# Optimization experiments

Measured on AMD Instinct MI355X. Metric: run time of the kernel, lower is better.

The kernel has to match this reference:

```python
import jax, jax.numpy as jnp
import numpy as np
from jax import lax

DIM = 64
D_STATE = 16
D_CONV = 4
EXPAND = 2
D_INNER = EXPAND * DIM  # 128
EPS = 1e-3  # keras LayerNormalization default epsilon


def setup_inputs() -> dict:
    key = jax.random.key(0)
    ks = jax.random.split(key, 9)
    B, H, W, D = 2, 48, 48, 48
    x = jax.random.normal(ks[0], (B, H, W, D, DIM), dtype=jnp.float32)
    # Dense kernels (fan-in scaled), conv kernel is depthwise: [k, 1, d_inner]
    W_in = jax.random.normal(ks[1], (DIM, 2 * D_INNER), jnp.float32) / np.sqrt(DIM)
    conv_w = jax.random.normal(ks[2], (D_CONV, 1, D_INNER), jnp.float32) / np.sqrt(D_CONV)
    conv_b = jnp.zeros((D_INNER,), jnp.float32)
    W_x = jax.random.normal(ks[3], (D_INNER, D_STATE + D_INNER), jnp.float32) / np.sqrt(D_INNER)
    W_dt = jax.random.normal(ks[4], (D_INNER, D_INNER), jnp.float32) / np.sqrt(D_INNER)
    b_dt = jnp.zeros((D_INNER,), jnp.float32)
    W_out = jax.random.normal(ks[5], (D_INNER, DIM), jnp.float32) / np.sqrt(D_INNER)
    gamma = jnp.ones((DIM,), jnp.float32)
    beta = jnp.zeros((DIM,), jnp.float32)
    return {"x": x, "W_in": W_in, "conv_w": conv_w, "conv_b": conv_b,
            "W_x": W_x, "W_dt": W_dt, "b_dt": b_dt, "W_out": W_out,
            "gamma": gamma, "beta": beta}


def _layernorm(z, gamma, beta):
    mu = jnp.mean(z, axis=-1, keepdims=True)
    var = jnp.mean(jnp.square(z - mu), axis=-1, keepdims=True)
    return gamma * (z - mu) * lax.rsqrt(var + EPS) + beta


def reference(x, W_in, conv_w, conv_b, W_x, W_dt, b_dt, W_out, gamma, beta):
    B, H, W, D, C = x.shape
    L = H * W * D
    x_flat = x.reshape(B, L, C)                       # [B, L, C]
    x_and_res = x_flat @ W_in                         # [B, L, 2*d_inner]
    x_ssm, res = jnp.split(x_and_res, 2, axis=-1)     # each [B, L, d_inner]
    # depthwise Conv1D, kernel=4, TF 'same' padding (pad_left=1, pad_right=2)
    x_ssm = lax.conv_general_dilated(
        x_ssm, conv_w, window_strides=(1,), padding=[(1, 2)],
        dimension_numbers=("NWC", "WIO", "NWC"), feature_group_count=D_INNER) + conv_b
    x_ssm = jax.nn.silu(x_ssm)
    # simplified SSM: projections + softplus + cumulative-sum scan over L
    x_proj = x_ssm @ W_x                              # [B, L, d_state+d_inner]
    dt = jax.nn.softplus(x_ssm @ W_dt + b_dt)         # [B, L, d_inner]
    state = jnp.cumsum(x_proj[..., :D_INNER] * dt, axis=1)  # [B, L, d_inner]
    y = state * jax.nn.silu(res)                      # gated output
    out = (y @ W_out).reshape(B, H, W, D, C)
    return _layernorm(out + x, gamma, beta)
```

## Files before the change

### kernel.cpp

```cpp
#include <hip/hip_runtime.h>
#include <hip/hip_bf16.h>
#include <math.h>

#define L_LEN 110592
#define TILE 32
#define NT 3456
#define NCH 64
#define TPC 54
#define STRX 72
#define STRC 136
#define RESS 132

typedef float  floatx4 __attribute__((ext_vector_type(4)));
typedef short  short8  __attribute__((ext_vector_type(8)));
typedef short  short4v __attribute__((ext_vector_type(4)));

__device__ __forceinline__ float fast_silu(float v) {
    return v * __builtin_amdgcn_rcpf(1.f + __expf(-v));
}
__device__ __forceinline__ float fast_softplus(float d) {
    return fmaxf(d, 0.f) + __logf(1.f + __expf(-fabsf(d)));
}
__device__ __forceinline__ short f2bf(float f) {
    __hip_bfloat16 h = __float2bfloat16(f);
    return *reinterpret_cast<short*>(&h);
}
__device__ __forceinline__ float bf2f(short s) {
    __hip_bfloat16 h = *reinterpret_cast<__hip_bfloat16*>(&s);
    return __bfloat162float(h);
}
__device__ __forceinline__ short8 pack_bf8(float4 a, float4 b) {
    short8 r;
    r[0] = f2bf(a.x); r[1] = f2bf(a.y); r[2] = f2bf(a.z); r[3] = f2bf(a.w);
    r[4] = f2bf(b.x); r[5] = f2bf(b.y); r[6] = f2bf(b.z); r[7] = f2bf(b.w);
    return r;
}

__global__ __launch_bounds__(256) void kW_w(
    const float* __restrict__ W_in, const float* __restrict__ W_x,
    const float* __restrict__ W_dt, const float* __restrict__ W_out,
    __hip_bfloat16* __restrict__ wti, __hip_bfloat16* __restrict__ wpt,
    __hip_bfloat16* __restrict__ wtr, __hip_bfloat16* __restrict__ wot)
{
    const int t = threadIdx.x;
    for (int idx = t; idx < 128 * 64; idx += 256) {
        int n = idx >> 6, k = idx & 63;
        wti[idx] = __float2bfloat16(W_in[k * 256 + n]);
        wtr[idx] = __float2bfloat16(W_in[k * 256 + 128 + n]);
    }
    for (int idx = t; idx < 256 * 128; idx += 256) {
        int n = idx >> 7, k = idx & 127;
        float v = (n < 128) ? W_x[k * 144 + n] : W_dt[k * 128 + (n - 128)];
        wpt[idx] = __float2bfloat16(v);
    }
    for (int idx = t; idx < 64 * 128; idx += 256) {
        int n = idx >> 7, k = idx & 127;
        wot[idx] = __float2bfloat16(W_out[k * 64 + n]);
    }
}

__global__ __launch_bounds__(256, 8) void kA(
    const float* __restrict__ x,
    const __hip_bfloat16* __restrict__ wti,
    const __hip_bfloat16* __restrict__ wpt,
    const float* __restrict__ conv_w, const float* __restrict__ conv_b,
    const float* __restrict__ b_dt,
    __hip_bfloat16* __restrict__ s, float* __restrict__ sums)
{
    __shared__ __align__(16) __hip_bfloat16 xbf[48 * STRX];
    __shared__ __align__(16) __hip_bfloat16 xcb[32 * STRC];

    const int t = threadIdx.x;
    const int lane = t & 63;
    const int w = t >> 6;
    const int quad = lane >> 4;
    const int lr = lane & 15;
    const int tile = blockIdx.x;
    const int b = blockIdx.y;
    const int l0 = tile * TILE;

    for (int idx = t; idx < 384; idx += 256) {
        const int row = idx >> 3, c8 = (idx & 7) << 3;
        const long gr = (long)l0 - 1 + row;
        float4 u0 = {0.f, 0.f, 0.f, 0.f}, u1 = {0.f, 0.f, 0.f, 0.f};
        if (gr >= 0 && gr < L_LEN) {
            const float* xp = x + (((long)b * L_LEN + gr) << 6) + c8;
            u0 = ((const float4*)xp)[0];
            u1 = ((const float4*)xp)[1];
        }
        *(short8*)&xbf[row * STRX + c8] = pack_bf8(u0, u1);
    }
    __syncthreads();

    {
        floatx4 acc[3][2] = {};
        #pragma unroll
        for (int ks = 0; ks < 2; ++ks) {
            short8 bfr0 = *(const short8*)(wti + ((w * 32 + lr) << 6) + ks * 32 + quad * 8);
            short8 bfr1 = *(const short8*)(wti + ((w * 32 + 16 + lr) << 6) + ks * 32 + quad * 8);
            #pragma unroll
            for (int mt = 0; mt < 3; ++mt) {
                short8 afr = *(const short8*)&xbf[(mt * 16 + lr) * STRX + ks * 32 + quad * 8];
                acc[mt][0] = __builtin_amdgcn_mfma_f32_16x16x32_bf16(afr, bfr0, acc[mt][0], 0, 0, 0);
                acc[mt][1] = __builtin_amdgcn_mfma_f32_16x16x32_bf16(afr, bfr1, acc[mt][1], 0, 0, 0);
            }
        }
        const int srcLane = (((quad + 1) & 3) << 4) | lr;
        #pragma unroll
        for (int jj = 0; jj < 2; ++jj) {
            const int col = w * 32 + jj * 16 + lr;
            const float cw0 = conv_w[col],       cw1 = conv_w[128 + col];
            const float cw2 = conv_w[256 + col], cw3 = conv_w[384 + col];
            const float cb = conv_b[col];
            #pragma unroll
            for (int m = 0; m < 2; ++m) {
                float s0 = (quad == 0) ? acc[m + 1][jj][0] : acc[m][jj][0];
                float s1 = (quad == 0) ? acc[m + 1][jj][1] : acc[m][jj][1];
                float s2 = (quad == 0) ? acc[m + 1][jj][2] : acc[m][jj][2];
                const float e0 = __shfl(s0, srcLane);
                const float e1 = __shfl(s1, srcLane);
                const float e2 = __shfl(s2, srcLane);
                const float a0 = acc[m][jj][0], a1 = acc[m][jj][1];
                const float a2 = acc[m][jj][2], a3 = acc[m][jj][3];
                const int rb = m * 16 + quad * 4;
                xcb[(rb + 0) * STRC + col] =
                    __float2bfloat16(fast_silu(cb + cw0 * a0 + cw1 * a1 + cw2 * a2 + cw3 * a3));
                xcb[(rb + 1) * STRC + col] =
                    __float2bfloat16(fast_silu(cb + cw0 * a1 + cw1 * a2 + cw2 * a3 + cw3 * e0));
                xcb[(rb + 2) * STRC + col] =
                    __float2bfloat16(fast_silu(cb + cw0 * a2 + cw1 * a3 + cw2 * e0 + cw3 * e1));
                xcb[(rb + 3) * STRC + col] =
                    __float2bfloat16(fast_silu(cb + cw0 * a3 + cw1 * e0 + cw2 * e1 + cw3 * e2));
            }
        }
    }
    __syncthreads();

    {
        floatx4 accx[2][2] = {}, accd[2][2] = {};
        #pragma unroll
        for (int ks = 0; ks < 4; ++ks) {
            short8 afr[2];
            #pragma unroll
            for (int mt = 0; mt < 2; ++mt)
                afr[mt] = *(const short8*)&xcb[(mt * 16 + lr) * STRC + ks * 32 + quad * 8];
            #pragma unroll
            for (int j = 0; j < 2; ++j) {
                const int n = w * 32 + j * 16 + lr;
                short8 bx = *(const short8*)(wpt + (n << 7) + ks * 32 + quad * 8);
                short8 bd = *(const short8*)(wpt + ((n + 128) << 7) + ks * 32 + quad * 8);
                #pragma unroll
                for (int mt = 0; mt < 2; ++mt) {
                    accx[mt][j] = __builtin_amdgcn_mfma_f32_16x16x32_bf16(afr[mt], bx, accx[mt][j], 0, 0, 0);
                    accd[mt][j] = __builtin_amdgcn_mfma_f32_16x16x32_bf16(afr[mt], bd, accd[mt][j], 0, 0, 0);
                }
            }
        }
        const long tbase = ((long)b * NT + tile) << 7;
        float ps0 = 0.f, ps1 = 0.f;
        #pragma unroll
        for (int j = 0; j < 2; ++j) {
            const int col = w * 32 + j * 16 + lr;
            const float bdv = b_dt[col];
            __hip_bfloat16* sp = s + ((tbase + col) << 5) + quad * 4;
            float psl = 0.f;
            #pragma unroll
            for (int mt = 0; mt < 2; ++mt) {
                short4v pk;
                #pragma unroll
                for (int r = 0; r < 4; ++r) {
                    float dv = accd[mt][j][r] + bdv;
                    float sv = accx[mt][j][r] * fast_softplus(dv);
                    short h = f2bf(sv);
                    pk[r] = h;
                    psl += bf2f(h);
                }
                *(short4v*)(sp + mt * 16) = pk;
            }
            if (j == 0) ps0 = psl; else ps1 = psl;
        }
        ps0 += __shfl_xor(ps0, 16); ps0 += __shfl_xor(ps0, 32);
        ps1 += __shfl_xor(ps1, 16); ps1 += __shfl_xor(ps1, 32);
        const long sb = ((long)b * NT + tile) << 7;
        if (quad == 0)      sums[sb + w * 32 + lr] = ps0;
        else if (quad == 1) sums[sb + w * 32 + 16 + lr] = ps1;
    }
}

__global__ __launch_bounds__(256) void kB1(const float* __restrict__ sums,
                                           float* __restrict__ csum)
{
    __shared__ float ps[256];
    const int t = threadIdx.x;
    const int c = t & 127, h = t >> 7;
    const int ch = blockIdx.x, b = blockIdx.y;
    const long tb = ((long)b * NT + ch * TPC + h * 27) * 128 + c;
    float tot = 0.f;
    for (int j = 0; j < 27; j += 9) {
        float v[9];
        #pragma unroll
        for (int k = 0; k < 9; ++k) v[k] = sums[tb + (long)(j + k) * 128];
        #pragma unroll
        for (int k = 0; k < 9; ++k) tot += v[k];
    }
    ps[t] = tot;
    __syncthreads();
    if (t < 128) csum[((long)b * NCH + ch) * 128 + t] = ps[t] + ps[t + 128];
}

__global__ __launch_bounds__(256) void kB2(float* __restrict__ csum)
{
    const int t = threadIdx.x;
    const int c = t & 127, b = t >> 7;
    const long base = (long)b * NCH * 128 + c;
    float run = 0.f;
    for (int ch = 0; ch < NCH; ch += 8) {
        float v[8];
        #pragma unroll
        for (int k = 0; k < 8; ++k) v[k] = csum[base + (long)(ch + k) * 128];
        #pragma unroll
        for (int k = 0; k < 8; ++k) {
            csum[base + (long)(ch + k) * 128] = run;
            run += v[k];
        }
    }
}

__global__ __launch_bounds__(128) void kB3(float* __restrict__ sums,
                                           const float* __restrict__ csum)
{
    const int c = threadIdx.x;
    const int ch = blockIdx.x, b = blockIdx.y;
    float run = csum[((long)b * NCH + ch) * 128 + c];
    const long tb = ((long)b * NT + ch * TPC) * 128 + c;
    for (int j = 0; j < TPC; j += 9) {
        float v[9];
        #pragma unroll
        for (int k = 0; k < 9; ++k) v[k] = sums[tb + (long)(j + k) * 128];
        #pragma unroll
        for (int k = 0; k < 9; ++k) {
            sums[tb + (long)(j + k) * 128] = run;
            run += v[k];
        }
    }
}

__global__ __launch_bounds__(256, 6) void kC(
    const float* __restrict__ x,
    const __hip_bfloat16* __restrict__ wtr,
    const __hip_bfloat16* __restrict__ wot,
    const float* __restrict__ gamma, const float* __restrict__ beta,
    const __hip_bfloat16* __restrict__ s, const float* __restrict__ offs,
    float* __restrict__ out)
{
    __shared__ float resf[32 * RESS];
    __shared__ __align__(16) char ubuf[32 * STRC * 2];
    __shared__ float totbuf[256];

    __hip_bfloat16* const ybf = (__hip_bfloat16*)ubuf;
    __hip_bfloat16* const xbf = (__hip_bfloat16*)ubuf;

    const int t = threadIdx.x;
    const int lane = t & 63;
    const int w = t >> 6;
    const int quad = lane >> 4;
    const int lr = lane & 15;
    const int tile = blockIdx.x;
    const int b = blockIdx.y;
    const int l0 = tile * TILE;
    const long base = (long)b * L_LEN;

    {
        const int row = t >> 3, c8 = (t & 7) << 3;
        const float* xp = x + ((base + l0 + row) << 6) + c8;
        float4 u0 = ((const float4*)xp)[0], u1 = ((const float4*)xp)[1];
        *(short8*)&xbf[row * STRX + c8] = pack_bf8(u0, u1);
    }
    __syncthreads();

    {
        floatx4 acc[2][2] = {};
        #pragma unroll
        for (int ks = 0; ks < 2; ++ks) {
            short8 bfr0 = *(const short8*)(wtr + ((w * 32 + lr) << 6) + ks * 32 + quad * 8);
            short8 bfr1 = *(const short8*)(wtr + ((w * 32 + 16 + lr) << 6) + ks * 32 + quad * 8);
            #pragma unroll
            for (int mt = 0; mt < 2; ++mt) {
                short8 afr = *(const short8*)&xbf[(mt * 16 + lr) * STRX + ks * 32 + quad * 8];
                acc[mt][0] = __builtin_amdgcn_mfma_f32_16x16x32_bf16(afr, bfr0, acc[mt][0], 0, 0, 0);
                acc[mt][1] = __builtin_amdgcn_mfma_f32_16x16x32_bf16(afr, bfr1, acc[mt][1], 0, 0, 0);
            }
        }
        #pragma unroll
        for (int mt = 0; mt < 2; ++mt)
            #pragma unroll
            for (int j = 0; j < 2; ++j) {
                const int col = w * 32 + j * 16 + lr;
                #pragma unroll
                for (int r = 0; r < 4; ++r)
                    resf[(mt * 16 + quad * 4 + r) * RESS + col] = fast_silu(acc[mt][j][r]);
            }
    }
    __syncthreads();

    {
        const int c = t & 127, h = t >> 7;
        const __hip_bfloat16* sp = s + ((((long)b * NT + tile) << 7) + c) * 32 + h * 16;
        short8 sv0 = *(const short8*)sp;
        short8 sv1 = *(const short8*)(sp + 8);
        float pfx[16];
        float run = 0.f;
        #pragma unroll
        for (int i = 0; i < 8; ++i) { run += bf2f(sv0[i]); pfx[i] = run; }
        #pragma unroll
        for (int i = 0; i < 8; ++i) { run += bf2f(sv1[i]); pfx[8 + i] = run; }
        totbuf[t] = run;
        __syncthreads();
        float off = offs[((long)b * NT + tile) * 128 + c];
        if (h) off += totbuf[c];
        #pragma unroll
        for (int q = 0; q < 16; ++q)
            ybf[(h * 16 + q) * STRC + c] =
                __float2bfloat16(resf[(h * 16 + q) * RESS + c] * (off + pfx[q]));
    }
    __syncthreads();

    {
        float* zbuf = resf;
        floatx4 acc[2] = {};
        const int n = w * 16 + lr;
        #pragma unroll
        for (int ks = 0; ks < 4; ++ks) {
            short8 bfr = *(const short8*)(wot + (n << 7) + ks * 32 + quad * 8);
            #pragma unroll
            for (int mt = 0; mt < 2; ++mt) {
                short8 afr = *(const short8*)&ybf[(mt * 16 + lr) * STRC + ks * 32 + quad * 8];
                acc[mt] = __builtin_amdgcn_mfma_f32_16x16x32_bf16(afr, bfr, acc[mt], 0, 0, 0);
            }
        }
        __syncthreads();
        #pragma unroll
        for (int mt = 0; mt < 2; ++mt)
            #pragma unroll
            for (int r = 0; r < 4; ++r)
                zbuf[(mt * 16 + quad * 4 + r) * 68 + n] = acc[mt][r];
    }
    __syncthreads();

    {
        const float* zbuf = resf;
        const int d = t & 63;
        const int dg = t >> 6;
        const float g  = gamma[d];
        const float bt = beta[d];
        #pragma unroll 2
        for (int i = 0; i < 8; ++i) {
            int q = dg + 4 * i;
            float z = zbuf[q * 68 + d] + x[(base + l0 + q) * 64 + d];
            float zsum = z;
            #pragma unroll
            for (int off = 32; off > 0; off >>= 1) zsum += __shfl_xor(zsum, off);
            float mu = zsum * 0.015625f;
            float dz = z - mu;
            float vsum = dz * dz;
            #pragma unroll
            for (int off = 32; off > 0; off >>= 1) vsum += __shfl_xor(vsum, off);
            float inv = rsqrtf(vsum * 0.015625f + 1e-3f);
            out[(base + l0 + q) * 64 + d] = g * dz * inv + bt;
        }
    }
}

extern "C" void kernel_launch(void* const* d_in, const int* in_sizes, int n_in,
                              void* d_out, int out_size, void* d_ws, size_t ws_size,
                              hipStream_t stream) {
    const float* x      = (const float*)d_in[0];
    const float* W_in   = (const float*)d_in[1];
    const float* conv_w = (const float*)d_in[2];
    const float* conv_b = (const float*)d_in[3];
    const float* W_x    = (const float*)d_in[4];
    const float* W_dt   = (const float*)d_in[5];
    const float* b_dt   = (const float*)d_in[6];
    const float* W_out  = (const float*)d_in[7];
    const float* gamma  = (const float*)d_in[8];
    const float* beta   = (const float*)d_in[9];
    float* out = (float*)d_out;

    __hip_bfloat16* s    = (__hip_bfloat16*)d_ws;
    float*          sums = (float*)((char*)d_ws + 56623104);
    float*          csum = (float*)((char*)d_ws + 60162048);
    __hip_bfloat16* wti  = (__hip_bfloat16*)((char*)d_ws + 88477696);
    __hip_bfloat16* wpt  = (__hip_bfloat16*)((char*)d_ws + 88494080);
    __hip_bfloat16* wtr  = (__hip_bfloat16*)((char*)d_ws + 88559616);
    __hip_bfloat16* wot  = (__hip_bfloat16*)((char*)d_ws + 88576000);

    kW_w<<<1, 256, 0, stream>>>(W_in, W_x, W_dt, W_out, wti, wpt, wtr, wot);
    dim3 grid(NT, 2);
    kA<<<grid, 256, 0, stream>>>(x, wti, wpt, conv_w, conv_b, b_dt, s, sums);
    dim3 gridB(NCH, 2);
    kB1<<<gridB, 256, 0, stream>>>(sums, csum);
    kB2<<<1, 256, 0, stream>>>(csum);
    kB3<<<gridB, 128, 0, stream>>>(sums, csum);
    kC<<<grid, 256, 0, stream>>>(x, wtr, wot, gamma, beta, s, sums, out);
}
```

Baseline: 283.4 us.

## Fuse pipeline into single kernel with decoupled look-back scan across tiles

Replaces the multi-kernel pipeline (projection kernel, three scan-offset kernels, output kernel) with one fused kernel. Each tile publishes its per-channel aggregate and, via flags, an inclusive prefix that later tiles read using a decoupled look-back. This removes the global round-trip of the bf16 state tensor and the extra launches, and x is read once instead of twice. The cost is a serial dependency chain between tiles that relies on blocks being scheduled roughly in order, spin-waiting, and lower occupancy from the larger shared memory footprint.

```diff
diff --git a/kernel.cpp b/kernel.cpp
--- a/kernel.cpp
+++ b/kernel.cpp
@@ -5,10 +5,9 @@
 #define L_LEN 110592
 #define TILE 32
 #define NT 3456
-#define NCH 64
-#define TPC 54
 #define STRX 72
 #define STRC 136
+#define STRS 40
 #define RESS 132
 
 typedef float  floatx4 __attribute__((ext_vector_type(4)));
@@ -40,7 +39,8 @@
     const float* __restrict__ W_in, const float* __restrict__ W_x,
     const float* __restrict__ W_dt, const float* __restrict__ W_out,
     __hip_bfloat16* __restrict__ wti, __hip_bfloat16* __restrict__ wpt,
-    __hip_bfloat16* __restrict__ wtr, __hip_bfloat16* __restrict__ wot)
+    __hip_bfloat16* __restrict__ wtr, __hip_bfloat16* __restrict__ wot,
+    int* __restrict__ flags)
 {
     const int t = threadIdx.x;
     for (int idx = t; idx < 128 * 64; idx += 256) {
@@ -57,18 +57,30 @@
         int n = idx >> 7, k = idx & 127;
         wot[idx] = __float2bfloat16(W_out[k * 64 + n]);
     }
-}
-
-__global__ __launch_bounds__(256, 8) void kA(
+    for (int idx = t; idx < 2 * NT; idx += 256) flags[idx] = 0;
+}
+
+__global__ __launch_bounds__(256, 4) void kF(
     const float* __restrict__ x,
     const __hip_bfloat16* __restrict__ wti,
     const __hip_bfloat16* __restrict__ wpt,
+    const __hip_bfloat16* __restrict__ wtr,
+    const __hip_bfloat16* __restrict__ wot,
     const float* __restrict__ conv_w, const float* __restrict__ conv_b,
     const float* __restrict__ b_dt,
-    __hip_bfloat16* __restrict__ s, float* __restrict__ sums)
+    const float* __restrict__ gamma, const float* __restrict__ beta,
+    float* __restrict__ agg, float* __restrict__ pref,
+    int* __restrict__ flags, float* __restrict__ out)
 {
-    __shared__ __align__(16) __hip_bfloat16 xbf[48 * STRX];
-    __shared__ __align__(16) __hip_bfloat16 xcb[32 * STRC];
+    __shared__ __align__(16) char pool[35584];
+    __hip_bfloat16* const xbf  = (__hip_bfloat16*)pool;
+    __hip_bfloat16* const xcb  = (__hip_bfloat16*)(pool + 6912);
+    __hip_bfloat16* const sbuf = (__hip_bfloat16*)(pool + 6912);
+    __hip_bfloat16* const ybf  = (__hip_bfloat16*)(pool + 6912);
+    float* const resf = (float*)(pool + 17152);
+    float* const totb = (float*)(pool + 34048);
+    float* const offb = totb;
+    float* const aggb = (float*)(pool + 35072);
 
     const int t = threadIdx.x;
     const int lane = t & 63;
@@ -78,13 +90,15 @@
     const int tile = blockIdx.x;
     const int b = blockIdx.y;
     const int l0 = tile * TILE;
+    const long base = (long)b * L_LEN;
+    const long cb = (long)b * NT;
 
     for (int idx = t; idx < 384; idx += 256) {
         const int row = idx >> 3, c8 = (idx & 7) << 3;
         const long gr = (long)l0 - 1 + row;
         float4 u0 = {0.f, 0.f, 0.f, 0.f}, u1 = {0.f, 0.f, 0.f, 0.f};
         if (gr >= 0 && gr < L_LEN) {
-            const float* xp = x + (((long)b * L_LEN + gr) << 6) + c8;
+            const float* xp = x + ((base + gr) << 6) + c8;
             u0 = ((const float4*)xp)[0];
             u1 = ((const float4*)xp)[1];
         }
@@ -111,7 +125,7 @@
             const int col = w * 32 + jj * 16 + lr;
             const float cw0 = conv_w[col],       cw1 = conv_w[128 + col];
             const float cw2 = conv_w[256 + col], cw3 = conv_w[384 + col];
-            const float cb = conv_b[col];
+            const float cbv = conv_b[col];
             #pragma unroll
             for (int m = 0; m < 2; ++m) {
                 float s0 = (quad == 0) ? acc[m + 1][jj][0] : acc[m][jj][0];
@@ -124,13 +138,13 @@
                 const float a2 = acc[m][jj][2], a3 = acc[m][jj][3];
                 const int rb = m * 16 + quad * 4;
                 xcb[(rb + 0) * STRC + col] =
-                    __float2bfloat16(fast_silu(cb + cw0 * a0 + cw1 * a1 + cw2 * a2 + cw3 * a3));
+                    __float2bfloat16(fast_silu(cbv + cw0 * a0 + cw1 * a1 + cw2 * a2 + cw3 * a3));
                 xcb[(rb + 1) * STRC + col] =
-                    __float2bfloat16(fast_silu(cb + cw0 * a1 + cw1 * a2 + cw2 * a3 + cw3 * e0));
+                    __float2bfloat16(fast_silu(cbv + cw0 * a1 + cw1 * a2 + cw2 * a3 + cw3 * e0));
                 xcb[(rb + 2) * STRC + col] =
-                    __float2bfloat16(fast_silu(cb + cw0 * a2 + cw1 * a3 + cw2 * e0 + cw3 * e1));
+                    __float2bfloat16(fast_silu(cbv + cw0 * a2 + cw1 * a3 + cw2 * e0 + cw3 * e1));
                 xcb[(rb + 3) * STRC + col] =
-                    __float2bfloat16(fast_silu(cb + cw0 * a3 + cw1 * e0 + cw2 * e1 + cw3 * e2));
+                    __float2bfloat16(fast_silu(cbv + cw0 * a3 + cw1 * e0 + cw2 * e1 + cw3 * e2));
             }
         }
     }
@@ -156,13 +170,13 @@
                 }
             }
         }
-        const long tbase = ((long)b * NT + tile) << 7;
+        __syncthreads();
+
         float ps0 = 0.f, ps1 = 0.f;
         #pragma unroll
         for (int j = 0; j < 2; ++j) {
             const int col = w * 32 + j * 16 + lr;
             const float bdv = b_dt[col];
-            __hip_bfloat16* sp = s + ((tbase + col) << 5) + quad * 4;
             float psl = 0.f;
             #pragma unroll
             for (int mt = 0; mt < 2; ++mt) {
@@ -175,108 +189,26 @@
                     pk[r] = h;
                     psl += bf2f(h);
                 }
-                *(short4v*)(sp + mt * 16) = pk;
+                *(short4v*)&sbuf[col * STRS + quad * 4 + mt * 16] = pk;
             }
             if (j == 0) ps0 = psl; else ps1 = psl;
         }
         ps0 += __shfl_xor(ps0, 16); ps0 += __shfl_xor(ps0, 32);
         ps1 += __shfl_xor(ps1, 16); ps1 += __shfl_xor(ps1, 32);
-        const long sb = ((long)b * NT + tile) << 7;
-        if (quad == 0)      sums[sb + w * 32 + lr] = ps0;
-        else if (quad == 1) sums[sb + w * 32 + 16 + lr] = ps1;
-    }
-}
-
-__global__ __launch_bounds__(256) void kB1(const float* __restrict__ sums,
-                                           float* __restrict__ csum)
-{
-    __shared__ float ps[256];
-    const int t = threadIdx.x;
-    const int c = t & 127, h = t >> 7;
-    const int ch = blockIdx.x, b = blockIdx.y;
-    const long tb = ((long)b * NT + ch * TPC + h * 27) * 128 + c;
-    float tot = 0.f;
-    for (int j = 0; j < 27; j += 9) {
-        float v[9];
-        #pragma unroll
-        for (int k = 0; k < 9; ++k) v[k] = sums[tb + (long)(j + k) * 128];
-        #pragma unroll
-        for (int k = 0; k < 9; ++k) tot += v[k];
-    }
-    ps[t] = tot;
-    __syncthreads();
-    if (t < 128) csum[((long)b * NCH + ch) * 128 + t] = ps[t] + ps[t + 128];
-}
-
-__global__ __launch_bounds__(256) void kB2(float* __restrict__ csum)
-{
-    const int t = threadIdx.x;
-    const int c = t & 127, b = t >> 7;
-    const long base = (long)b * NCH * 128 + c;
-    float run = 0.f;
-    for (int ch = 0; ch < NCH; ch += 8) {
-        float v[8];
-        #pragma unroll
-        for (int k = 0; k < 8; ++k) v[k] = csum[base + (long)(ch + k) * 128];
-        #pragma unroll
-        for (int k = 0; k < 8; ++k) {
-            csum[base + (long)(ch + k) * 128] = run;
-            run += v[k];
-        }
-    }
-}
-
-__global__ __launch_bounds__(128) void kB3(float* __restrict__ sums,
-                                           const float* __restrict__ csum)
-{
-    const int c = threadIdx.x;
-    const int ch = blockIdx.x, b = blockIdx.y;
-    float run = csum[((long)b * NCH + ch) * 128 + c];
-    const long tb = ((long)b * NT + ch * TPC) * 128 + c;
-    for (int j = 0; j < TPC; j += 9) {
-        float v[9];
-        #pragma unroll
-        for (int k = 0; k < 9; ++k) v[k] = sums[tb + (long)(j + k) * 128];
-        #pragma unroll
-        for (int k = 0; k < 9; ++k) {
-            sums[tb + (long)(j + k) * 128] = run;
-            run += v[k];
-        }
-    }
-}
-
-__global__ __launch_bounds__(256, 6) void kC(
-    const float* __restrict__ x,
-    const __hip_bfloat16* __restrict__ wtr,
-    const __hip_bfloat16* __restrict__ wot,
-    const float* __restrict__ gamma, const float* __restrict__ beta,
-    const __hip_bfloat16* __restrict__ s, const float* __restrict__ offs,
-    float* __restrict__ out)
-{
-    __shared__ float resf[32 * RESS];
-    __shared__ __align__(16) char ubuf[32 * STRC * 2];
-    __shared__ float totbuf[256];
-
-    __hip_bfloat16* const ybf = (__hip_bfloat16*)ubuf;
-    __hip_bfloat16* const xbf = (__hip_bfloat16*)ubuf;
-
-    const int t = threadIdx.x;
-    const int lane = t & 63;
-    const int w = t >> 6;
-    const int quad = lane >> 4;
-    const int lr = lane & 15;
-    const int tile = blockIdx.x;
-    const int b = blockIdx.y;
-    const int l0 = tile * TILE;
-    const long base = (long)b * L_LEN;
-
-    {
-        const int row = t >> 3, c8 = (t & 7) << 3;
-        const float* xp = x + ((base + l0 + row) << 6) + c8;
-        float4 u0 = ((const float4*)xp)[0], u1 = ((const float4*)xp)[1];
-        *(short8*)&xbf[row * STRX + c8] = pack_bf8(u0, u1);
-    }
-    __syncthreads();
+        const long mb = (cb + tile) << 7;
+        if (quad == 0) {
+            const int col = w * 32 + lr;
+            aggb[col] = ps0;
+            __hip_atomic_store(&agg[mb + col], ps0, __ATOMIC_RELAXED, __HIP_MEMORY_SCOPE_AGENT);
+        } else if (quad == 1) {
+            const int col = w * 32 + 16 + lr;
+            aggb[col] = ps1;
+            __hip_atomic_store(&agg[mb + col], ps1, __ATOMIC_RELAXED, __HIP_MEMORY_SCOPE_AGENT);
+        }
+        __syncthreads();
+        if (t == 0)
+            __hip_atomic_store(&flags[cb + tile], 1, __ATOMIC_RELEASE, __HIP_MEMORY_SCOPE_AGENT);
+    }
 
     {
         floatx4 acc[2][2] = {};
@@ -286,7 +218,7 @@
             short8 bfr1 = *(const short8*)(wtr + ((w * 32 + 16 + lr) << 6) + ks * 32 + quad * 8);
             #pragma unroll
             for (int mt = 0; mt < 2; ++mt) {
-                short8 afr = *(const short8*)&xbf[(mt * 16 + lr) * STRX + ks * 32 + quad * 8];
+                short8 afr = *(const short8*)&xbf[(1 + mt * 16 + lr) * STRX + ks * 32 + quad * 8];
                 acc[mt][0] = __builtin_amdgcn_mfma_f32_16x16x32_bf16(afr, bfr0, acc[mt][0], 0, 0, 0);
                 acc[mt][1] = __builtin_amdgcn_mfma_f32_16x16x32_bf16(afr, bfr1, acc[mt][1], 0, 0, 0);
             }
@@ -301,27 +233,68 @@
                     resf[(mt * 16 + quad * 4 + r) * RESS + col] = fast_silu(acc[mt][j][r]);
             }
     }
-    __syncthreads();
-
-    {
-        const int c = t & 127, h = t >> 7;
-        const __hip_bfloat16* sp = s + ((((long)b * NT + tile) << 7) + c) * 32 + h * 16;
-        short8 sv0 = *(const short8*)sp;
-        short8 sv1 = *(const short8*)(sp + 8);
-        float pfx[16];
+
+    const int c = t & 127, hh = t >> 7;
+    float pfx[16];
+    float offl;
+    {
+        short8 sv0 = *(const short8*)&sbuf[c * STRS + hh * 16];
+        short8 sv1 = *(const short8*)&sbuf[c * STRS + hh * 16 + 8];
         float run = 0.f;
         #pragma unroll
         for (int i = 0; i < 8; ++i) { run += bf2f(sv0[i]); pfx[i] = run; }
         #pragma unroll
         for (int i = 0; i < 8; ++i) { run += bf2f(sv1[i]); pfx[8 + i] = run; }
-        totbuf[t] = run;
+        totb[t] = run;
         __syncthreads();
-        float off = offs[((long)b * NT + tile) * 128 + c];
-        if (h) off += totbuf[c];
+        offl = hh ? totb[c] : 0.f;
+    }
+    __syncthreads();
+
+    if (w == 0) {
+        float o0 = 0.f, o1 = 0.f;
+        int p = tile - 1;
+        while (p >= 0) {
+            const int W = (p + 1 < 64) ? (p + 1) : 64;
+            int fl = 0;
+            if (lane < W)
+                fl = __hip_atomic_load(&flags[cb + p - lane], __ATOMIC_ACQUIRE, __HIP_MEMORY_SCOPE_AGENT);
+            const unsigned long long m2 = __ballot(fl == 2);
+            const unsigned long long m0 = __ballot(fl == 0);
+            const int k2 = m2 ? (__ffsll(m2) - 1) : 64;
+            const int k0 = m0 ? (__ffsll(m0) - 1) : 64;
+            const bool hp = (k2 < k0);
+            const int usable = hp ? k2 : k0;
+            for (int q = 0; q < usable; ++q) {
+                const long pb = (cb + (p - q)) << 7;
+                o0 += __hip_atomic_load(&agg[pb + lane], __ATOMIC_RELAXED, __HIP_MEMORY_SCOPE_AGENT);
+                o1 += __hip_atomic_load(&agg[pb + 64 + lane], __ATOMIC_RELAXED, __HIP_MEMORY_SCOPE_AGENT);
+            }
+            if (hp) {
+                const long pb = (cb + (p - usable)) << 7;
+                o0 += __hip_atomic_load(&pref[pb + lane], __ATOMIC_RELAXED, __HIP_MEMORY_SCOPE_AGENT);
+                o1 += __hip_atomic_load(&pref[pb + 64 + lane], __ATOMIC_RELAXED, __HIP_MEMORY_SCOPE_AGENT);
+                break;
+            }
+            p -= usable;
+            if (usable == 0) __builtin_amdgcn_s_sleep(8);
+        }
+        const long mb = (cb + tile) << 7;
+        __hip_atomic_store(&pref[mb + lane], o0 + aggb[lane], __ATOMIC_RELAXED, __HIP_MEMORY_SCOPE_AGENT);
+        __hip_atomic_store(&pref[mb + 64 + lane], o1 + aggb[lane + 64], __ATOMIC_RELAXED, __HIP_MEMORY_SCOPE_AGENT);
+        if (lane == 0)
+            __hip_atomic_store(&flags[cb + tile], 2, __ATOMIC_RELEASE, __HIP_MEMORY_SCOPE_AGENT);
+        offb[lane] = o0;
+        offb[lane + 64] = o1;
+    }
+    __syncthreads();
+
+    {
+        const float off = offb[c] + offl;
         #pragma unroll
         for (int q = 0; q < 16; ++q)
-            ybf[(h * 16 + q) * STRC + c] =
-                __float2bfloat16(resf[(h * 16 + q) * RESS + c] * (off + pfx[q]));
+            ybf[(hh * 16 + q) * STRC + c] =
+                __float2bfloat16(resf[(hh * 16 + q) * RESS + c] * (off + pfx[q]));
     }
     __syncthreads();
 
@@ -386,20 +359,16 @@
     const float* beta   = (const float*)d_in[9];
     float* out = (float*)d_out;
 
-    __hip_bfloat16* s    = (__hip_bfloat16*)d_ws;
-    float*          sums = (float*)((char*)d_ws + 56623104);
-    float*          csum = (float*)((char*)d_ws + 60162048);
-    __hip_bfloat16* wti  = (__hip_bfloat16*)((char*)d_ws + 88477696);
-    __hip_bfloat16* wpt  = (__hip_bfloat16*)((char*)d_ws + 88494080);
-    __hip_bfloat16* wtr  = (__hip_bfloat16*)((char*)d_ws + 88559616);
-    __hip_bfloat16* wot  = (__hip_bfloat16*)((char*)d_ws + 88576000);
-
-    kW_w<<<1, 256, 0, stream>>>(W_in, W_x, W_dt, W_out, wti, wpt, wtr, wot);
+    float* agg   = (float*)d_ws;
+    float* pref  = (float*)((char*)d_ws + 3538944);
+    int*   flags = (int*)((char*)d_ws + 7077888);
+    __hip_bfloat16* wti = (__hip_bfloat16*)((char*)d_ws + 8000000);
+    __hip_bfloat16* wpt = (__hip_bfloat16*)((char*)d_ws + 8016384);
+    __hip_bfloat16* wtr = (__hip_bfloat16*)((char*)d_ws + 8081920);
+    __hip_bfloat16* wot = (__hip_bfloat16*)((char*)d_ws + 8098304);
+
+    kW_w<<<1, 256, 0, stream>>>(W_in, W_x, W_dt, W_out, wti, wpt, wtr, wot, flags);
     dim3 grid(NT, 2);
-    kA<<<grid, 256, 0, stream>>>(x, wti, wpt, conv_w, conv_b, b_dt, s, sums);
-    dim3 gridB(NCH, 2);
-    kB1<<<gridB, 256, 0, stream>>>(sums, csum);
-    kB2<<<1, 256, 0, stream>>>(csum);
-    kB3<<<gridB, 128, 0, stream>>>(sums, csum);
-    kC<<<grid, 256, 0, stream>>>(x, wtr, wot, gamma, beta, s, sums, out);
-}
+    kF<<<grid, 256, 0, stream>>>(x, wti, wpt, wtr, wot, conv_w, conv_b, b_dt,
+                                 gamma, beta, agg, pref, flags, out);
+}
```

Measured after the change: 725.9 us. +156.1%, slower.
